# Kernel tuning notes

Measured on AMD Instinct MI355X. Metric: run time of the kernel, lower is better.

## Reference

```python
import jax, jax.numpy as jnp
import numpy as np


def setup_inputs() -> dict:
    key = jax.random.key(0)
    ks = jax.random.split(key, 5)
    B, L, C = 32, 64, 128      # batch, set_size, input_channels
    D, O = 512, 256            # mlp hidden dim, output_channels
    L2 = L * L                 # 4096 = set_size**2 (FSPool set size)
    x = jax.random.normal(ks[0], (B, L, C), dtype=jnp.float32)
    # Linear weights stored as [in, out]; kaiming-ish scaling
    w1 = jax.random.normal(ks[1], (2 * C, D), dtype=jnp.float32) / np.sqrt(2 * C)
    b1 = jnp.zeros((D,), dtype=jnp.float32)
    w2 = jax.random.normal(ks[2], (D, O), dtype=jnp.float32) / np.sqrt(D)
    b2 = jnp.zeros((O,), dtype=jnp.float32)
    # FSPool weight [set_size**2, out_channels], kaiming_normal fan_out linear
    pool_w = jax.random.normal(ks[3], (L2, O), dtype=jnp.float32) / np.sqrt(O)
    return {"x": x, "w1": w1, "b1": b1, "w2": w2, "b2": b2, "pool_w": pool_w}


def reference(x, w1, b1, w2, b2, pool_w):
    B, L, C = x.shape
    # create_pairs + concat: [B, L, L, 2C] -> flatten to [B, L*L, 2C]
    a = jnp.broadcast_to(x[:, :, None, :], (B, L, L, C))
    b = jnp.broadcast_to(x[:, None, :, :], (B, L, L, C))
    pairs = jnp.concatenate([a, b], axis=-1).reshape(B, L * L, 2 * C)
    # 2-layer MLP
    h = jax.nn.relu(pairs @ w1 + b1)            # [B, L^2, D]
    y = h @ w2 + b2                             # [B, L^2, O]
    # FSPool: featurewise sort over set dim, then weighted sum
    y = jnp.sort(y, axis=1)                     # [B, L^2, O]
    return jnp.einsum('nlc,lc->nc', y, pool_w)  # [B, O]
```

## Files before the change

### kernel.cpp

```cpp
#include <hip/hip_runtime.h>
#include <hip/hip_bf16.h>
#include <hip/hip_fp16.h>

typedef __attribute__((ext_vector_type(4))) float f32x4;
typedef _Float16 h8 __attribute__((ext_vector_type(8)));
typedef int i32x4 __attribute__((ext_vector_type(4)));
typedef _Float16 h2 __attribute__((ext_vector_type(2)));

static __device__ __forceinline__ h2 ih2(int x) { return __builtin_bit_cast(h2, x); }
static __device__ __forceinline__ unsigned pkrtz(float lo, float hi) {
  return __builtin_bit_cast(unsigned, __builtin_amdgcn_cvt_pkrtz(lo, hi));
}
static __device__ __forceinline__ int pkmin(int x, int y) {
  int d; asm("v_pk_min_f16 %0, %1, %2" : "=v"(d) : "v"(x), "v"(y)); return d;
}
static __device__ __forceinline__ int pkmax(int x, int y) {
  int d; asm("v_pk_max_f16 %0, %1, %2" : "=v"(d) : "v"(x), "v"(y)); return d;
}
static __device__ __forceinline__ int pkadd(int x, int y) {
  int d; asm("v_pk_add_f16 %0, %1, %2" : "=v"(d) : "v"(x), "v"(y)); return d;
}


__global__ __launch_bounds__(256) void k_uv(const float* __restrict__ x,
                                            const float* __restrict__ w1,
                                            const float* __restrict__ b1,
                                            _Float16* __restrict__ u,
                                            _Float16* __restrict__ v) {
  __shared__ float xs[8 * 128];
  int t = threadIdx.x;
  int r0 = blockIdx.x * 8;
  ((float4*)xs)[t] = ((const float4*)(x + (size_t)r0 * 128))[t];
  __syncthreads();
  int d1 = t, d2 = t + 256;
  float au0[8], au1[8], av0[8], av1[8];
  float bb1 = b1[d1], bb2 = b1[d2];
#pragma unroll
  for (int r = 0; r < 8; ++r) { au0[r] = bb1; au1[r] = bb2; av0[r] = 0.f; av1[r] = 0.f; }
#pragma unroll 4
  for (int c = 0; c < 128; ++c) {
    float wu1 = w1[c * 512 + d1];
    float wu2 = w1[c * 512 + d2];
    float wv1 = w1[(c + 128) * 512 + d1];
    float wv2 = w1[(c + 128) * 512 + d2];
#pragma unroll
    for (int r = 0; r < 8; ++r) {
      float xv = xs[r * 128 + c];
      au0[r] = fmaf(xv, wu1, au0[r]);
      au1[r] = fmaf(xv, wu2, au1[r]);
      av0[r] = fmaf(xv, wv1, av0[r]);
      av1[r] = fmaf(xv, wv2, av1[r]);
    }
  }
#pragma unroll
  for (int r = 0; r < 8; ++r) {
    u[(size_t)(r0 + r) * 512 + d1] = (_Float16)au0[r];
    u[(size_t)(r0 + r) * 512 + d2] = (_Float16)au1[r];
    v[(size_t)(r0 + r) * 512 + d1] = (_Float16)av0[r];
    v[(size_t)(r0 + r) * 512 + d2] = (_Float16)av1[r];
  }
}

__global__ __launch_bounds__(256) void k_w2t(const float* __restrict__ w2,
                                             _Float16* __restrict__ w2t) {
  int n = blockIdx.x;
  int t = threadIdx.x;
  w2t[(size_t)n * 512 + t]       = (_Float16)w2[(size_t)t * 256 + n];
  w2t[(size_t)n * 512 + t + 256] = (_Float16)w2[(size_t)(t + 256) * 256 + n];
}

__global__ __launch_bounds__(256) void k_pwt(const float* __restrict__ pw,
                                             float* __restrict__ pwt) {
  int o = blockIdx.x;
  int t = threadIdx.x;
#pragma unroll
  for (int it = 0; it < 16; ++it) {
    int l = it * 256 + t;
    pwt[(size_t)o * 4096 + l] = pw[(size_t)l * 256 + o];
  }
}

__global__ __launch_bounds__(256, 2) void k_gemm(const _Float16* __restrict__ u,
                                                 const _Float16* __restrict__ v,
                                                 const _Float16* __restrict__ w2t,
                                                 const float* __restrict__ b2,
                                                 unsigned short* __restrict__ yt) {
  __shared__ char vl[64 * 1024];
  __shared__ char ulm[4 * 1024];
  int t = threadIdx.x;
  int n0 = blockIdx.x;
  int bid = (n0 & 7) * 64 + (n0 >> 3);
  int b = bid >> 4, ig = bid & 15;
  {
    const char* vsrc = (const char*)(v + (size_t)b * 64 * 512);
#pragma unroll
    for (int it = 0; it < 16; ++it) {
      int f = it * 4096 + t * 16;
      uint4 d = *(const uint4*)(vsrc + f);
      int row = f >> 10;
      *(uint4*)(vl + (f ^ ((row & 7) << 4))) = d;
    }
    const char* usrc = (const char*)(u + (size_t)(b * 64 + ig * 4) * 512);
    int f = t * 16;
    *(uint4*)(ulm + f) = *(const uint4*)(usrc + f);
  }
  __syncthreads();
  int w = t >> 6, l = t & 63, lr = l & 15, lg = l >> 4;
  const _Float16* bptr[4];
  float bias[4];
#pragma unroll
  for (int ni = 0; ni < 4; ++ni) {
    int col = w * 64 + ni * 16 + lr;
    bptr[ni] = w2t + (size_t)col * 512 + lg * 8;
    bias[ni] = b2[col];
  }
#pragma unroll 1
  for (int ih = 0; ih < 2; ++ih) {
    f32x4 acc[2][4][4];
#pragma unroll
    for (int ip = 0; ip < 2; ++ip)
#pragma unroll
      for (int mi = 0; mi < 4; ++mi)
#pragma unroll
        for (int ni = 0; ni < 4; ++ni) {
          float bv = bias[ni];
          f32x4 ci = {bv, bv, bv, bv};
          acc[ip][mi][ni] = ci;
        }
#pragma unroll 2
    for (int kk = 0; kk < 16; ++kk) {
      h8 bfv[4];
#pragma unroll
      for (int ni = 0; ni < 4; ++ni) bfv[ni] = *(const h8*)(bptr[ni] + kk * 32);
      i32x4 vf[4];
#pragma unroll
      for (int mi = 0; mi < 4; ++mi) {
        int row = mi * 16 + lr;
        int fb = row * 1024 + kk * 64 + lg * 16;
        vf[mi] = *(const i32x4*)(vl + (fb ^ ((row & 7) << 4)));
      }
#pragma unroll
      for (int ip = 0; ip < 2; ++ip) {
        i32x4 uf = *(const i32x4*)(ulm + (ih * 2 + ip) * 1024 + kk * 64 + lg * 16);
#pragma unroll
        for (int mi = 0; mi < 4; ++mi) {
          i32x4 aw;
#pragma unroll
          for (int q = 0; q < 4; ++q) aw[q] = pkmax(pkadd(uf[q], vf[mi][q]), 0);
          h8 af = __builtin_bit_cast(h8, aw);
#pragma unroll
          for (int ni = 0; ni < 4; ++ni)
            acc[ip][mi][ni] =
                __builtin_amdgcn_mfma_f32_16x16x32_f16(af, bfv[ni], acc[ip][mi][ni], 0, 0, 0);
        }
      }
    }
#pragma unroll
    for (int ip = 0; ip < 2; ++ip) {
      int i = ig * 4 + ih * 2 + ip;
#pragma unroll
      for (int ni = 0; ni < 4; ++ni) {
        int col = w * 64 + ni * 16 + lr;
        unsigned short* colbase = yt + (size_t)(b * 256 + col) * 4096 + (size_t)i * 64;
#pragma unroll
        for (int mi = 0; mi < 4; ++mi) {
          f32x4 vv = acc[ip][mi][ni];
          uint2 st;
          st.x = pkrtz(vv[0], vv[1]);
          st.y = pkrtz(vv[2], vv[3]);
          *(uint2*)(colbase + mi * 16 + lg * 4) = st;
        }
      }
    }
  }
}

template <int M, int HB>
static __device__ __forceinline__ void intra(int* a) {
#pragma unroll
  for (int e = 0; e < 16; ++e)
    if ((e & HB) == 0) {
      int f = e ^ M;
      int lo = pkmin(a[e], a[f]);
      int hi = pkmax(a[e], a[f]);
      a[e] = lo;
      a[f] = hi;
    }
}

template <int CTRL, bool FLIP>
static __device__ __forceinline__ void xdpp(int* a, bool km) {
  int r[16];
#pragma unroll
  for (int e = 0; e < 16; ++e)
    r[e] = __builtin_amdgcn_mov_dpp(a[FLIP ? (e ^ 15) : e], CTRL, 0xf, 0xf, true);
#pragma unroll
  for (int e = 0; e < 16; ++e) a[e] = km ? pkmin(a[e], r[e]) : pkmax(a[e], r[e]);
}
#define DPP_X1 0xB1
#define DPP_X2 0x4E
#define DPP_X3 0x1B
#define DPP_X7 0x141
#define DPP_X8 0x128
#define DPP_XF 0x140

template <bool FLIP>
static __device__ __forceinline__ void xw(int* a, int tm, bool km, int l) {
  int paddr = (l ^ tm) << 2;
  int r[16];
#pragma unroll
  for (int e = 0; e < 16; ++e)
    r[e] = __builtin_amdgcn_ds_bpermute(paddr, a[FLIP ? (e ^ 15) : e]);
#pragma unroll
  for (int e = 0; e < 16; ++e) a[e] = km ? pkmin(a[e], r[e]) : pkmax(a[e], r[e]);
}

template <bool FLIP>
static __device__ __forceinline__ void xl(int* a, int tm, bool km, int t, int* sl) {
  __syncthreads();
#pragma unroll
  for (int e = 0; e < 16; ++e) sl[e * 256 + t] = a[e];
  __syncthreads();
  int pt = t ^ tm;
  int r[16];
#pragma unroll
  for (int e = 0; e < 16; ++e) r[e] = sl[(FLIP ? (e ^ 15) : e) * 256 + pt];
#pragma unroll
  for (int e = 0; e < 16; ++e) a[e] = km ? pkmin(a[e], r[e]) : pkmax(a[e], r[e]);
}

__global__ __launch_bounds__(256) void k_sortpool(const unsigned short* __restrict__ yt,
                                                  const float* __restrict__ pwt,
                                                  float* __restrict__ out) {
  __shared__ int sl[4096];
  __shared__ float red[8];
  int t = threadIdx.x;
  int l = t & 63;
  int b = blockIdx.x >> 7, p = blockIdx.x & 127;
  int o0 = p * 2, o1 = p * 2 + 1;
  const uint4* c0 = (const uint4*)(yt + (size_t)(b * 256 + o0) * 4096 + t * 16);
  const uint4* c1 = (const uint4*)(yt + (size_t)(b * 256 + o1) * 4096 + t * 16);
  uint4 A0 = c0[0], A1 = c0[1], B0 = c1[0], B1 = c1[1];
  unsigned cw0[8] = {A0.x, A0.y, A0.z, A0.w, A1.x, A1.y, A1.z, A1.w};
  unsigned cw1[8] = {B0.x, B0.y, B0.z, B0.w, B1.x, B1.y, B1.z, B1.w};
  int a[16];
#pragma unroll
  for (int q = 0; q < 8; ++q) {
    a[2 * q]     = (int)((cw0[q] & 0xffffu) | (cw1[q] << 16));
    a[2 * q + 1] = (int)((cw0[q] >> 16) | (cw1[q] & 0xffff0000u));
  }
  intra<1, 1>(a);
  intra<3, 2>(a); intra<1, 1>(a);
  intra<7, 4>(a); intra<2, 2>(a); intra<1, 1>(a);
  intra<15, 8>(a); intra<4, 4>(a); intra<2, 2>(a); intra<1, 1>(a);
#define INTRA4 intra<8, 8>(a); intra<4, 4>(a); intra<2, 2>(a); intra<1, 1>(a)
  xdpp<DPP_X1, true>(a, !(t & 1)); INTRA4;
  xdpp<DPP_X3, true>(a, !(t & 2)); xdpp<DPP_X1, false>(a, !(t & 1)); INTRA4;
  xdpp<DPP_X7, true>(a, !(t & 4)); xdpp<DPP_X2, false>(a, !(t & 2));
  xdpp<DPP_X1, false>(a, !(t & 1)); INTRA4;
  xdpp<DPP_XF, true>(a, !(t & 8)); xw<false>(a, 4, !(t & 4), l);
  xdpp<DPP_X2, false>(a, !(t & 2)); xdpp<DPP_X1, false>(a, !(t & 1)); INTRA4;
  xw<true>(a, 31, !(t & 16), l); xdpp<DPP_X8, false>(a, !(t & 8));
  xw<false>(a, 4, !(t & 4), l); xdpp<DPP_X2, false>(a, !(t & 2));
  xdpp<DPP_X1, false>(a, !(t & 1)); INTRA4;
  xw<true>(a, 63, !(t & 32), l); xw<false>(a, 16, !(t & 16), l);
  xdpp<DPP_X8, false>(a, !(t & 8)); xw<false>(a, 4, !(t & 4), l);
  xdpp<DPP_X2, false>(a, !(t & 2)); xdpp<DPP_X1, false>(a, !(t & 1)); INTRA4;
  xl<true>(a, 127, !(t & 64), t, sl);
  xw<false>(a, 32, !(t & 32), l); xw<false>(a, 16, !(t & 16), l);
  xdpp<DPP_X8, false>(a, !(t & 8)); xw<false>(a, 4, !(t & 4), l);
  xdpp<DPP_X2, false>(a, !(t & 2)); xdpp<DPP_X1, false>(a, !(t & 1)); INTRA4;
  xl<true>(a, 255, !(t & 128), t, sl);
  xl<false>(a, 64, !(t & 64), t, sl);
  xw<false>(a, 32, !(t & 32), l); xw<false>(a, 16, !(t & 16), l);
  xdpp<DPP_X8, false>(a, !(t & 8)); xw<false>(a, 4, !(t & 4), l);
  xdpp<DPP_X2, false>(a, !(t & 2)); xdpp<DPP_X1, false>(a, !(t & 1)); INTRA4;
#undef INTRA4
  const float* pw0 = pwt + (size_t)o0 * 4096 + t * 16;
  const float* pw1 = pwt + (size_t)o1 * 4096 + t * 16;
  float s0 = 0.f, s1 = 0.f;
#pragma unroll
  for (int e = 0; e < 16; ++e) {
    h2 v2 = ih2(a[e]);
    s0 = fmaf((float)v2[0], pw0[e], s0);
    s1 = fmaf((float)v2[1], pw1[e], s1);
  }
#pragma unroll
  for (int off = 32; off > 0; off >>= 1) {
    s0 += __shfl_xor(s0, off);
    s1 += __shfl_xor(s1, off);
  }
  int wv = t >> 6;
  if (l == 0) { red[wv * 2] = s0; red[wv * 2 + 1] = s1; }
  __syncthreads();
  if (t == 0) out[b * 256 + o0] = red[0] + red[2] + red[4] + red[6];
  if (t == 1) out[b * 256 + o1] = red[1] + red[3] + red[5] + red[7];
}

extern "C" void kernel_launch(void* const* d_in, const int* in_sizes, int n_in,
                              void* d_out, int out_size, void* d_ws, size_t ws_size,
                              hipStream_t stream) {
  const float* x  = (const float*)d_in[0];
  const float* w1 = (const float*)d_in[1];
  const float* b1 = (const float*)d_in[2];
  const float* w2 = (const float*)d_in[3];
  const float* b2 = (const float*)d_in[4];
  const float* pw = (const float*)d_in[5];
  char* ws = (char*)d_ws;
  _Float16* u   = (_Float16*)ws;
  _Float16* v   = (_Float16*)(ws + (2u << 20));
  _Float16* w2t = (_Float16*)(ws + (4u << 20));
  float*    pwt = (float*)(ws + (5u << 20));
  unsigned short* yt = (unsigned short*)(ws + (9u << 20));
  float* out = (float*)d_out;

  k_uv<<<dim3(256), dim3(256), 0, stream>>>(x, w1, b1, u, v);
  k_w2t<<<dim3(256), dim3(256), 0, stream>>>(w2, w2t);
  k_pwt<<<dim3(256), dim3(256), 0, stream>>>(pw, pwt);
  k_gemm<<<dim3(512), dim3(256), 0, stream>>>(u, v, w2t, b2, yt);
  k_sortpool<<<dim3(4096), dim3(256), 0, stream>>>(yt, pwt, out);
}
```

Baseline: 171.5 us.

## Sort each column pair within one wavefront holding 64 elements per lane

The sort-pool kernel shrinks from 256 threads to a single 64-lane wavefront, with each lane holding 64 packed fp16 pairs instead of 16. The bitonic network now runs more in-register stages and uses only DPP and ds_bpermute exchanges. This removes the LDS stages, the __syncthreads barriers and the cross-wave reduction. In exchange register pressure rises sharply (64-element arrays per lane), which lowers occupancy and may cause spills.

```diff
diff --git a/kernel.cpp b/kernel.cpp
--- a/kernel.cpp
+++ b/kernel.cpp
@@ -175,10 +175,17 @@
   }
 }
 
+#define DPP_X1 0xB1
+#define DPP_X2 0x4E
+#define DPP_X3 0x1B
+#define DPP_X7 0x141
+#define DPP_X8 0x128
+#define DPP_XF 0x140
+
 template <int M, int HB>
 static __device__ __forceinline__ void intra(int* a) {
 #pragma unroll
-  for (int e = 0; e < 16; ++e)
+  for (int e = 0; e < 64; ++e)
     if ((e & HB) == 0) {
       int f = e ^ M;
       int lo = pkmin(a[e], a[f]);
@@ -188,113 +195,117 @@
     }
 }
 
-template <int CTRL, bool FLIP>
-static __device__ __forceinline__ void xdpp(int* a, bool km) {
-  int r[16];
-#pragma unroll
-  for (int e = 0; e < 16; ++e)
-    r[e] = __builtin_amdgcn_mov_dpp(a[FLIP ? (e ^ 15) : e], CTRL, 0xf, 0xf, true);
-#pragma unroll
-  for (int e = 0; e < 16; ++e) a[e] = km ? pkmin(a[e], r[e]) : pkmax(a[e], r[e]);
-}
-#define DPP_X1 0xB1
-#define DPP_X2 0x4E
-#define DPP_X3 0x1B
-#define DPP_X7 0x141
-#define DPP_X8 0x128
-#define DPP_XF 0x140
-
-template <bool FLIP>
-static __device__ __forceinline__ void xw(int* a, int tm, bool km, int l) {
-  int paddr = (l ^ tm) << 2;
-  int r[16];
-#pragma unroll
-  for (int e = 0; e < 16; ++e)
-    r[e] = __builtin_amdgcn_ds_bpermute(paddr, a[FLIP ? (e ^ 15) : e]);
-#pragma unroll
-  for (int e = 0; e < 16; ++e) a[e] = km ? pkmin(a[e], r[e]) : pkmax(a[e], r[e]);
-}
-
-template <bool FLIP>
-static __device__ __forceinline__ void xl(int* a, int tm, bool km, int t, int* sl) {
-  __syncthreads();
-#pragma unroll
-  for (int e = 0; e < 16; ++e) sl[e * 256 + t] = a[e];
-  __syncthreads();
-  int pt = t ^ tm;
-  int r[16];
-#pragma unroll
-  for (int e = 0; e < 16; ++e) r[e] = sl[(FLIP ? (e ^ 15) : e) * 256 + pt];
-#pragma unroll
-  for (int e = 0; e < 16; ++e) a[e] = km ? pkmin(a[e], r[e]) : pkmax(a[e], r[e]);
-}
-
-__global__ __launch_bounds__(256) void k_sortpool(const unsigned short* __restrict__ yt,
-                                                  const float* __restrict__ pwt,
-                                                  float* __restrict__ out) {
-  __shared__ int sl[4096];
-  __shared__ float red[8];
-  int t = threadIdx.x;
-  int l = t & 63;
+template <int CTRL>
+static __device__ __forceinline__ void cdpp(int* a, bool km) {
+#pragma unroll
+  for (int e = 0; e < 64; ++e) {
+    int r = __builtin_amdgcn_mov_dpp(a[e], CTRL, 0xf, 0xf, true);
+    int mn = pkmin(a[e], r), mx = pkmax(a[e], r);
+    a[e] = km ? mn : mx;
+  }
+}
+
+template <int CTRL>
+static __device__ __forceinline__ void fdpp(int* a, bool km) {
+#pragma unroll
+  for (int e = 0; e < 32; ++e) {
+    int f = e ^ 63;
+    int r0 = __builtin_amdgcn_mov_dpp(a[f], CTRL, 0xf, 0xf, true);
+    int r1 = __builtin_amdgcn_mov_dpp(a[e], CTRL, 0xf, 0xf, true);
+    int mn0 = pkmin(a[e], r0), mx0 = pkmax(a[e], r0);
+    int mn1 = pkmin(a[f], r1), mx1 = pkmax(a[f], r1);
+    a[e] = km ? mn0 : mx0;
+    a[f] = km ? mn1 : mx1;
+  }
+}
+
+static __device__ __forceinline__ void cbp(int* a, int tm, bool km, int t) {
+  int paddr = ((t ^ tm) & 63) << 2;
+#pragma unroll
+  for (int e = 0; e < 64; ++e) {
+    int r = __builtin_amdgcn_ds_bpermute(paddr, a[e]);
+    int mn = pkmin(a[e], r), mx = pkmax(a[e], r);
+    a[e] = km ? mn : mx;
+  }
+}
+
+static __device__ __forceinline__ void fbp(int* a, int tm, bool km, int t) {
+  int paddr = ((t ^ tm) & 63) << 2;
+#pragma unroll
+  for (int e = 0; e < 32; ++e) {
+    int f = e ^ 63;
+    int r0 = __builtin_amdgcn_ds_bpermute(paddr, a[f]);
+    int r1 = __builtin_amdgcn_ds_bpermute(paddr, a[e]);
+    int mn0 = pkmin(a[e], r0), mx0 = pkmax(a[e], r0);
+    int mn1 = pkmin(a[f], r1), mx1 = pkmax(a[f], r1);
+    a[e] = km ? mn0 : mx0;
+    a[f] = km ? mn1 : mx1;
+  }
+}
+
+__global__ __launch_bounds__(64) void k_sortpool(const unsigned short* __restrict__ yt,
+                                                 const float* __restrict__ pwt,
+                                                 float* __restrict__ out) {
+  int t = threadIdx.x;
   int b = blockIdx.x >> 7, p = blockIdx.x & 127;
-  int o0 = p * 2, o1 = p * 2 + 1;
-  const uint4* c0 = (const uint4*)(yt + (size_t)(b * 256 + o0) * 4096 + t * 16);
-  const uint4* c1 = (const uint4*)(yt + (size_t)(b * 256 + o1) * 4096 + t * 16);
-  uint4 A0 = c0[0], A1 = c0[1], B0 = c1[0], B1 = c1[1];
-  unsigned cw0[8] = {A0.x, A0.y, A0.z, A0.w, A1.x, A1.y, A1.z, A1.w};
-  unsigned cw1[8] = {B0.x, B0.y, B0.z, B0.w, B1.x, B1.y, B1.z, B1.w};
-  int a[16];
+  int o0 = p * 2, o1 = o0 + 1;
+  const uint4* c0 = (const uint4*)(yt + (size_t)(b * 256 + o0) * 4096 + t * 64);
+  const uint4* c1 = (const uint4*)(yt + (size_t)(b * 256 + o1) * 4096 + t * 64);
+  int a[64];
 #pragma unroll
   for (int q = 0; q < 8; ++q) {
-    a[2 * q]     = (int)((cw0[q] & 0xffffu) | (cw1[q] << 16));
-    a[2 * q + 1] = (int)((cw0[q] >> 16) | (cw1[q] & 0xffff0000u));
+    uint4 x0 = c0[q], x1 = c1[q];
+    unsigned w0[4] = {x0.x, x0.y, x0.z, x0.w};
+    unsigned w1[4] = {x1.x, x1.y, x1.z, x1.w};
+#pragma unroll
+    for (int r = 0; r < 4; ++r) {
+      a[q * 8 + 2 * r]     = (int)((w0[r] & 0xffffu) | (w1[r] << 16));
+      a[q * 8 + 2 * r + 1] = (int)((w0[r] >> 16) | (w1[r] & 0xffff0000u));
+    }
   }
   intra<1, 1>(a);
   intra<3, 2>(a); intra<1, 1>(a);
   intra<7, 4>(a); intra<2, 2>(a); intra<1, 1>(a);
   intra<15, 8>(a); intra<4, 4>(a); intra<2, 2>(a); intra<1, 1>(a);
-#define INTRA4 intra<8, 8>(a); intra<4, 4>(a); intra<2, 2>(a); intra<1, 1>(a)
-  xdpp<DPP_X1, true>(a, !(t & 1)); INTRA4;
-  xdpp<DPP_X3, true>(a, !(t & 2)); xdpp<DPP_X1, false>(a, !(t & 1)); INTRA4;
-  xdpp<DPP_X7, true>(a, !(t & 4)); xdpp<DPP_X2, false>(a, !(t & 2));
-  xdpp<DPP_X1, false>(a, !(t & 1)); INTRA4;
-  xdpp<DPP_XF, true>(a, !(t & 8)); xw<false>(a, 4, !(t & 4), l);
-  xdpp<DPP_X2, false>(a, !(t & 2)); xdpp<DPP_X1, false>(a, !(t & 1)); INTRA4;
-  xw<true>(a, 31, !(t & 16), l); xdpp<DPP_X8, false>(a, !(t & 8));
-  xw<false>(a, 4, !(t & 4), l); xdpp<DPP_X2, false>(a, !(t & 2));
-  xdpp<DPP_X1, false>(a, !(t & 1)); INTRA4;
-  xw<true>(a, 63, !(t & 32), l); xw<false>(a, 16, !(t & 16), l);
-  xdpp<DPP_X8, false>(a, !(t & 8)); xw<false>(a, 4, !(t & 4), l);
-  xdpp<DPP_X2, false>(a, !(t & 2)); xdpp<DPP_X1, false>(a, !(t & 1)); INTRA4;
-  xl<true>(a, 127, !(t & 64), t, sl);
-  xw<false>(a, 32, !(t & 32), l); xw<false>(a, 16, !(t & 16), l);
-  xdpp<DPP_X8, false>(a, !(t & 8)); xw<false>(a, 4, !(t & 4), l);
-  xdpp<DPP_X2, false>(a, !(t & 2)); xdpp<DPP_X1, false>(a, !(t & 1)); INTRA4;
-  xl<true>(a, 255, !(t & 128), t, sl);
-  xl<false>(a, 64, !(t & 64), t, sl);
-  xw<false>(a, 32, !(t & 32), l); xw<false>(a, 16, !(t & 16), l);
-  xdpp<DPP_X8, false>(a, !(t & 8)); xw<false>(a, 4, !(t & 4), l);
-  xdpp<DPP_X2, false>(a, !(t & 2)); xdpp<DPP_X1, false>(a, !(t & 1)); INTRA4;
-#undef INTRA4
-  const float* pw0 = pwt + (size_t)o0 * 4096 + t * 16;
-  const float* pw1 = pwt + (size_t)o1 * 4096 + t * 16;
+  intra<31, 16>(a); intra<8, 8>(a); intra<4, 4>(a); intra<2, 2>(a); intra<1, 1>(a);
+  intra<63, 32>(a); intra<16, 16>(a); intra<8, 8>(a); intra<4, 4>(a);
+  intra<2, 2>(a); intra<1, 1>(a);
+#define CLEAN6 intra<32, 32>(a); intra<16, 16>(a); intra<8, 8>(a); \
+               intra<4, 4>(a); intra<2, 2>(a); intra<1, 1>(a)
+  fdpp<DPP_X1>(a, !(t & 1)); CLEAN6;
+  fdpp<DPP_X3>(a, !(t & 2)); cdpp<DPP_X1>(a, !(t & 1)); CLEAN6;
+  fdpp<DPP_X7>(a, !(t & 4)); cdpp<DPP_X2>(a, !(t & 2)); cdpp<DPP_X1>(a, !(t & 1)); CLEAN6;
+  fdpp<DPP_XF>(a, !(t & 8)); cbp(a, 4, !(t & 4), t);
+  cdpp<DPP_X2>(a, !(t & 2)); cdpp<DPP_X1>(a, !(t & 1)); CLEAN6;
+  fbp(a, 31, !(t & 16), t); cdpp<DPP_X8>(a, !(t & 8)); cbp(a, 4, !(t & 4), t);
+  cdpp<DPP_X2>(a, !(t & 2)); cdpp<DPP_X1>(a, !(t & 1)); CLEAN6;
+  fbp(a, 63, !(t & 32), t); cbp(a, 16, !(t & 16), t); cdpp<DPP_X8>(a, !(t & 8));
+  cbp(a, 4, !(t & 4), t); cdpp<DPP_X2>(a, !(t & 2)); cdpp<DPP_X1>(a, !(t & 1)); CLEAN6;
+#undef CLEAN6
+  const float4* pw0 = (const float4*)(pwt + (size_t)o0 * 4096 + t * 64);
+  const float4* pw1 = (const float4*)(pwt + (size_t)o1 * 4096 + t * 64);
   float s0 = 0.f, s1 = 0.f;
 #pragma unroll
-  for (int e = 0; e < 16; ++e) {
-    h2 v2 = ih2(a[e]);
-    s0 = fmaf((float)v2[0], pw0[e], s0);
-    s1 = fmaf((float)v2[1], pw1[e], s1);
+  for (int q = 0; q < 16; ++q) {
+    float4 w0 = pw0[q], w1 = pw1[q];
+    float k0[4] = {w0.x, w0.y, w0.z, w0.w};
+    float k1[4] = {w1.x, w1.y, w1.z, w1.w};
+#pragma unroll
+    for (int r = 0; r < 4; ++r) {
+      h2 v2 = ih2(a[q * 4 + r]);
+      s0 = fmaf((float)v2[0], k0[r], s0);
+      s1 = fmaf((float)v2[1], k1[r], s1);
+    }
   }
 #pragma unroll
   for (int off = 32; off > 0; off >>= 1) {
     s0 += __shfl_xor(s0, off);
     s1 += __shfl_xor(s1, off);
   }
-  int wv = t >> 6;
-  if (l == 0) { red[wv * 2] = s0; red[wv * 2 + 1] = s1; }
-  __syncthreads();
-  if (t == 0) out[b * 256 + o0] = red[0] + red[2] + red[4] + red[6];
-  if (t == 1) out[b * 256 + o1] = red[1] + red[3] + red[5] + red[7];
+  if (t == 0) {
+    out[b * 256 + o0] = s0;
+    out[b * 256 + o1] = s1;
+  }
 }
 
 extern "C" void kernel_launch(void* const* d_in, const int* in_sizes, int n_in,
@@ -318,5 +329,5 @@
   k_w2t<<<dim3(256), dim3(256), 0, stream>>>(w2, w2t);
   k_pwt<<<dim3(256), dim3(256), 0, stream>>>(pw, pwt);
   k_gemm<<<dim3(512), dim3(256), 0, stream>>>(u, v, w2t, b2, yt);
-  k_sortpool<<<dim3(4096), dim3(256), 0, stream>>>(yt, pwt, out);
-}
+  k_sortpool<<<dim3(4096), dim3(64), 0, stream>>>(yt, pwt, out);
+}
```

Result: faster. 153.1 us (-10.7%).
